# Optimization experiments

Measured on AMD Instinct MI355X. Metric: run time of the kernel, lower is better.

The kernel has to match this reference:

```python
import jax, jax.numpy as jnp
import numpy as np

DIM = 128; D_STATE = 16; D_CONV = 4; EXPAND = 2
D_INNER = DIM * EXPAND            # 256
DT_RANK = (DIM + 15) // 16        # 8
B, H, W = 2, 56, 56


def _ln(x, w, b):
    m = jnp.mean(x, -1, keepdims=True)
    v = jnp.var(x, -1, keepdims=True)
    return (x - m) * jax.lax.rsqrt(v + 1e-5) * w + b


def _mamba(x, in_w, conv_w, conv_b, xproj_w, dt_w, dt_b, A_log, Dp, out_w):
    # x: (B, L, DIM)
    Bb, L, _ = x.shape
    xz = x @ in_w.T                                   # (B,L,2*D_INNER)
    xi, z = jnp.split(xz, 2, axis=-1)
    # causal depthwise conv1d (pad left d_conv-1, truncate to L)
    xc = jnp.transpose(xi, (0, 2, 1))                 # (B,D_INNER,L)
    xc = jax.lax.conv_general_dilated(
        xc, conv_w, (1,), [(D_CONV - 1, 0)],
        dimension_numbers=('NCH', 'OIH', 'NCH'),
        feature_group_count=D_INNER) + conv_b[None, :, None]
    xs = jax.nn.silu(jnp.transpose(xc, (0, 2, 1)))    # (B,L,D_INNER)
    dbl = xs @ xproj_w.T                              # (B,L,DT_RANK+2*D_STATE)
    dt = jax.nn.softplus(dbl[..., :DT_RANK] @ dt_w.T + dt_b)   # (B,L,D_INNER)
    Bc = dbl[..., DT_RANK:DT_RANK + D_STATE]          # (B,L,D_STATE)
    Cc = dbl[..., DT_RANK + D_STATE:]                 # (B,L,D_STATE)
    A = -jnp.exp(A_log)                               # (D_INNER,D_STATE)
    dA = jnp.exp(dt[..., None] * A)                   # (B,L,D_INNER,D_STATE)
    dBu = (dt * xs)[..., None] * Bc[:, :, None, :]    # (B,L,D_INNER,D_STATE)

    def step(h, inp):
        a, bu, c = inp
        h = a * h + bu                                # (B,D_INNER,D_STATE)
        return h, jnp.einsum('bdn,bn->bd', h, c)

    h0 = jnp.zeros((Bb, D_INNER, D_STATE), x.dtype)
    _, ys = jax.lax.scan(step, h0, (jnp.moveaxis(dA, 1, 0),
                                    jnp.moveaxis(dBu, 1, 0),
                                    jnp.moveaxis(Cc, 1, 0)))
    y = jnp.moveaxis(ys, 0, 1) + xs * Dp              # (B,L,D_INNER)
    y = y * jax.nn.silu(z)
    return y @ out_w.T                                # (B,L,DIM)


def _forward(x, norm_h_w, norm_h_b, norm_v_w, norm_v_b,
             dw_w, dw_b, pw_w, pw_b,
             h_in_w, h_conv_w, h_conv_b, h_xproj_w, h_dt_w, h_dt_b, h_A_log, h_D, h_out_w,
             v_in_w, v_conv_w, v_conv_b, v_xproj_w, v_dt_w, v_dt_b, v_A_log, v_D, v_out_w,
             ca_fc1_w, ca_fc2_w):
    Bb, C, Hh, Ww = x.shape
    # local branch: depthwise 3x3 + GELU + 1x1
    lf = jax.lax.conv_general_dilated(
        x, dw_w, (1, 1), [(1, 1), (1, 1)],
        dimension_numbers=('NCHW', 'OIHW', 'NCHW'),
        feature_group_count=C) + dw_b[None, :, None, None]
    lf = jax.nn.gelu(lf, approximate=False)
    lf = jnp.einsum('bchw,oc->bohw', lf, pw_w[:, :, 0, 0]) + pw_b[None, :, None, None]
    # horizontal scan: row-major tokens
    xh = _ln(x.reshape(Bb, C, Hh * Ww).transpose(0, 2, 1), norm_h_w, norm_h_b)
    oh = _mamba(xh, h_in_w, h_conv_w, h_conv_b, h_xproj_w, h_dt_w, h_dt_b,
                h_A_log, h_D, h_out_w)
    oh = oh.transpose(0, 2, 1).reshape(Bb, C, Hh, Ww)
    # vertical scan: column-major tokens
    xv = _ln(jnp.transpose(x, (0, 1, 3, 2)).reshape(Bb, C, Ww * Hh).transpose(0, 2, 1),
             norm_v_w, norm_v_b)
    ov = _mamba(xv, v_in_w, v_conv_w, v_conv_b, v_xproj_w, v_dt_w, v_dt_b,
                v_A_log, v_D, v_out_w)
    ov = jnp.transpose(ov.transpose(0, 2, 1).reshape(Bb, C, Ww, Hh), (0, 1, 3, 2))
    fused = oh + ov + lf
    # channel attention
    y = jnp.mean(fused, axis=(2, 3))                  # (B,C)
    y = jax.nn.sigmoid(jax.nn.relu(y @ ca_fc1_w.T) @ ca_fc2_w.T)
    return fused * y[:, :, None, None] + x


def setup_inputs() -> dict:
    key = jax.random.key(0)
    ks = iter(jax.random.split(key, 64))
    def nrm(shape, scale):
        return jax.random.normal(next(ks), shape, jnp.float32) * scale
    d = {}
    d['x'] = nrm((B, DIM, H, W), 1.0)
    d['norm_h_w'] = jnp.ones((DIM,), jnp.float32); d['norm_h_b'] = jnp.zeros((DIM,), jnp.float32)
    d['norm_v_w'] = jnp.ones((DIM,), jnp.float32); d['norm_v_b'] = jnp.zeros((DIM,), jnp.float32)
    d['dw_w'] = nrm((DIM, 1, 3, 3), 1.0 / 3.0)
    d['dw_b'] = jnp.zeros((DIM,), jnp.float32)
    d['pw_w'] = nrm((DIM, DIM, 1, 1), DIM ** -0.5)
    d['pw_b'] = jnp.zeros((DIM,), jnp.float32)
    for p in ('h', 'v'):
        d[p + '_in_w'] = nrm((2 * D_INNER, DIM), DIM ** -0.5)
        d[p + '_conv_w'] = nrm((D_INNER, 1, D_CONV), D_CONV ** -0.5)
        d[p + '_conv_b'] = jnp.zeros((D_INNER,), jnp.float32)
        d[p + '_xproj_w'] = nrm((DT_RANK + 2 * D_STATE, D_INNER), D_INNER ** -0.5)
        d[p + '_dt_w'] = nrm((D_INNER, DT_RANK), DT_RANK ** -0.5)
        d[p + '_dt_b'] = jnp.full((D_INNER,), -2.0, jnp.float32)  # small positive dt
        d[p + '_A_log'] = jnp.log(jnp.tile(jnp.arange(1, D_STATE + 1, dtype=jnp.float32), (D_INNER, 1)))
        d[p + '_D'] = jnp.ones((D_INNER,), jnp.float32)
        d[p + '_out_w'] = nrm((DIM, D_INNER), D_INNER ** -0.5)
    d['ca_fc1_w'] = nrm((DIM // 4, DIM), DIM ** -0.5)
    d['ca_fc2_w'] = nrm((DIM, DIM // 4), (DIM // 4) ** -0.5)
    return d


def reference(x, norm_h_w, norm_h_b, norm_v_w, norm_v_b,
              dw_w, dw_b, pw_w, pw_b,
              h_in_w, h_conv_w, h_conv_b, h_xproj_w, h_dt_w, h_dt_b, h_A_log, h_D, h_out_w,
              v_in_w, v_conv_w, v_conv_b, v_xproj_w, v_dt_w, v_dt_b, v_A_log, v_D, v_out_w,
              ca_fc1_w, ca_fc2_w):
    return _forward(x, norm_h_w, norm_h_b, norm_v_w, norm_v_b,
                    dw_w, dw_b, pw_w, pw_b,
                    h_in_w, h_conv_w, h_conv_b, h_xproj_w, h_dt_w, h_dt_b, h_A_log, h_D, h_out_w,
                    v_in_w, v_conv_w, v_conv_b, v_xproj_w, v_dt_w, v_dt_b, v_A_log, v_D, v_out_w,
                    ca_fc1_w, ca_fc2_w)
```

## Files before the change

### kernel.cpp

```cpp
#include <hip/hip_runtime.h>
#include <hip/hip_bf16.h>

typedef __hip_bfloat16 bf16;
__device__ __forceinline__ float b2f(bf16 v){ return __bfloat162float(v); }
__device__ __forceinline__ bf16 f2b(float v){ return __float2bfloat16(v); }

typedef __attribute__((ext_vector_type(8))) short frag_ab;
typedef __attribute__((ext_vector_type(4))) float frag_cd;
typedef __attribute__((ext_vector_type(4))) short short4v;

__device__ __forceinline__ frag_ab ld_frag_2xb64(const bf16* p){
  union { frag_ab f; short4v h[2]; } u;
  u.h[0] = *reinterpret_cast<const short4v*>(p);
  u.h[1] = *reinterpret_cast<const short4v*>(p+4);
  return u.f;
}

#define LLEN 3136
#define BATCH 2
#define NCHUNK 49
#define LC 64

__global__ void k_dwconv_gelu(const float* __restrict__ x, const float* __restrict__ dww,
                              const float* __restrict__ dwb, bf16* __restrict__ tmp){
  int bc = blockIdx.x;
  int c = bc & 127;
  const float* xp = x + (size_t)bc*LLEN;
  float w[9];
  #pragma unroll
  for (int i=0;i<9;i++) w[i] = dww[c*9+i];
  float bias = dwb[c];
  for (int p = threadIdx.x; p < LLEN; p += blockDim.x){
    int i = p/56, j = p%56;
    float acc = bias;
    #pragma unroll
    for (int a=0;a<3;a++){
      int ii = i + a - 1;
      if (ii < 0 || ii >= 56) continue;
      #pragma unroll
      for (int bb=0;bb<3;bb++){
        int jj = j + bb - 1;
        if (jj < 0 || jj >= 56) continue;
        acc += w[a*3+bb] * xp[ii*56+jj];
      }
    }
    float g = 0.5f*acc*(1.0f + erff(acc*0.70710678118654752f));
    tmp[(size_t)bc*LLEN + p] = f2b(g);
  }
}

__global__ void k_pw_gemm(const bf16* __restrict__ tmp, const float* __restrict__ pww,
                          const float* __restrict__ pwb, float* __restrict__ fused){
  int b  = blockIdx.z;
  int p0 = blockIdx.x * 64;
  int m0 = blockIdx.y * 64;
  const bf16* T = tmp + (size_t)b*128*LLEN;
  __shared__ __align__(16) bf16 sA[64][136];
  __shared__ __align__(16) bf16 sBt[64][132];
  int tid = threadIdx.x;
  #pragma unroll
  for (int r=0;r<8;r++){
    int idx = tid + r*256;
    int row = idx >> 5, c4 = (idx & 31)*4;
    float4 w4 = *reinterpret_cast<const float4*>(&pww[(size_t)(m0+row)*128 + c4]);
    bf16 t4[4] = {f2b(w4.x), f2b(w4.y), f2b(w4.z), f2b(w4.w)};
    *reinterpret_cast<double*>(&sA[row][c4]) = *reinterpret_cast<double*>(t4);
  }
  #pragma unroll
  for (int r=0;r<8;r++){
    int idx = tid + r*256;
    int c = idx >> 4, p4 = (idx & 15)*4;
    union { double d; bf16 v[4]; } u;
    u.d = *reinterpret_cast<const double*>(&T[(size_t)c*LLEN + p0 + p4]);
    #pragma unroll
    for (int j=0;j<4;j++) sBt[p4+j][c] = u.v[j];
  }
  __syncthreads();
  int wv2 = tid >> 6, lane = tid & 63;
  int qd = lane >> 4, mr = lane & 15;
  frag_cd acc[4] = {};
  #pragma unroll
  for (int k0=0;k0<128;k0+=32){
    frag_ab af = *reinterpret_cast<frag_ab*>(&sA[wv2*16+mr][k0+qd*8]);
    #pragma unroll
    for (int t=0;t<4;t++){
      frag_ab bfr = ld_frag_2xb64(&sBt[t*16+mr][k0+qd*8]);
      acc[t] = __builtin_amdgcn_mfma_f32_16x16x32_bf16(af, bfr, acc[t], 0, 0, 0);
    }
  }
  #pragma unroll
  for (int t=0;t<4;t++)
    #pragma unroll
    for (int r=0;r<4;r++){
      int m = m0 + wv2*16 + qd*4 + r;
      int p = p0 + t*16 + mr;
      fused[((size_t)b*128 + m)*LLEN + p] = acc[t][r] + pwb[m];
    }
}

__global__ void k_ln(const float* __restrict__ x, const float* nhw_, const float* nhb_,
                     const float* nvw_, const float* nvb_, bf16* __restrict__ xln){
  __shared__ float sx[128][57];
  __shared__ float smean[56], srstd[56];
  __shared__ float wh[128], bh[128], wv_[128], bv_[128];
  int h = blockIdx.x; int b = blockIdx.y;
  int tid = threadIdx.x;
  if (tid < 128){ wh[tid]=nhw_[tid]; bh[tid]=nhb_[tid];
                  wv_[tid]=nvw_[tid]; bv_[tid]=nvb_[tid]; }
  for (int idx = tid; idx < 128*56; idx += 256){
    int c = idx / 56, w = idx % 56;
    sx[c][w] = x[((size_t)(b*128+c))*LLEN + h*56 + w];
  }
  __syncthreads();
  if (tid < 56){
    float s=0.f, s2=0.f;
    for (int c=0;c<128;c++){ float v = sx[c][tid]; s+=v; s2+=v*v; }
    float m = s*(1.f/128.f);
    float var = s2*(1.f/128.f) - m*m;
    smean[tid]=m; srstd[tid]=rsqrtf(var+1e-5f);
  }
  __syncthreads();
  bf16* outh = xln;
  bf16* outv = xln + (size_t)BATCH*LLEN*128;
  for (int idx = tid; idx < 56*128; idx += 256){
    int w = idx >> 7, c = idx & 127;
    float v = (sx[c][w]-smean[w])*srstd[w];
    outh[((size_t)b*LLEN + h*56 + w)*128 + c] = f2b(v*wh[c]+bh[c]);
    outv[((size_t)b*LLEN + w*56 + h)*128 + c] = f2b(v*wv_[c]+bv_[c]);
  }
}

__global__ void k_inproj(const bf16* __restrict__ xln, const float* __restrict__ hw,
                         const float* __restrict__ vw, bf16* __restrict__ XI, bf16* __restrict__ Z){
  int dir = blockIdx.z;
  const bf16* A = xln + (size_t)dir*BATCH*LLEN*128;
  const float* W = dir ? vw : hw;
  int m0 = blockIdx.x*64, n0 = blockIdx.y*64;
  __shared__ __align__(16) bf16 sA[64][136];
  __shared__ __align__(16) bf16 sW[64][136];
  int tid = threadIdx.x;
  #pragma unroll
  for (int r=0;r<4;r++){
    int idx = tid + r*256;
    int row = idx >> 4, c8 = (idx & 15)*8;
    *reinterpret_cast<float4*>(&sA[row][c8]) =
        *reinterpret_cast<const float4*>(&A[(size_t)(m0+row)*128 + c8]);
  }
  #pragma unroll
  for (int r=0;r<8;r++){
    int idx = tid + r*256;
    int row = idx >> 5, c4 = (idx & 31)*4;
    float4 w4 = *reinterpret_cast<const float4*>(&W[(size_t)(n0+row)*128 + c4]);
    bf16 t4[4] = {f2b(w4.x), f2b(w4.y), f2b(w4.z), f2b(w4.w)};
    *reinterpret_cast<double*>(&sW[row][c4]) = *reinterpret_cast<double*>(t4);
  }
  __syncthreads();
  int wv2 = tid >> 6, lane = tid & 63;
  int qd = lane >> 4, mr = lane & 15;
  frag_cd acc[4] = {};
  #pragma unroll
  for (int k0=0;k0<128;k0+=32){
    frag_ab af = *reinterpret_cast<frag_ab*>(&sA[wv2*16+mr][k0+qd*8]);
    #pragma unroll
    for (int t=0;t<4;t++){
      frag_ab bfr = *reinterpret_cast<frag_ab*>(&sW[t*16+mr][k0+qd*8]);
      acc[t] = __builtin_amdgcn_mfma_f32_16x16x32_bf16(af, bfr, acc[t], 0, 0, 0);
    }
  }
  bf16* dst = (n0 < 256) ? XI : Z;
  int nb = n0 & 255;
  size_t dslab = (size_t)dir*BATCH*LLEN*256;
  #pragma unroll
  for (int t=0;t<4;t++)
    #pragma unroll
    for (int r=0;r<4;r++){
      int row = m0 + wv2*16 + qd*4 + r;
      int col = nb + t*16 + mr;
      dst[dslab + (size_t)row*256 + col] = f2b(acc[t][r]);
    }
}

__global__ void k_conv(const bf16* __restrict__ XI, const float* hw, const float* hb,
                       const float* vw, const float* vb, bf16* __restrict__ XS2){
  int dir = blockIdx.z;
  int b = blockIdx.y;
  int bd = dir*BATCH + b;
  int l0 = blockIdx.x * 32;
  const bf16* XId = XI + (size_t)bd*LLEN*256;
  const float* cw = dir ? vw : hw;
  const float* cb = dir ? vb : hb;
  __shared__ float sxi[35][256];
  int tid = threadIdx.x;
  for (int r = 0; r < 35; r++){
    int l = l0 - 3 + r;
    sxi[r][tid] = (l >= 0) ? b2f(XId[(size_t)l*256 + tid]) : 0.f;
  }
  __syncthreads();
  float w0=cw[tid*4], w1=cw[tid*4+1], w2=cw[tid*4+2], w3=cw[tid*4+3];
  float bias = cb[tid];
  size_t x2base = ((size_t)bd*16 + (tid>>4))*LLEN;
  int c16 = tid & 15;
  for (int ll=0; ll<32; ll++){
    float acc = bias + w0*sxi[ll][tid] + w1*sxi[ll+1][tid] + w2*sxi[ll+2][tid] + w3*sxi[ll+3][tid];
    float s = acc / (1.f + __expf(-acc));
    XS2[(x2base + l0 + ll)*16 + c16] = f2b(s);
  }
}

__global__ void k_dbl(const bf16* __restrict__ XS2, const float* __restrict__ hx,
                      const float* __restrict__ vx,
                      const float* hdw, const float* vdw, const float* hdb, const float* vdb,
                      bf16* __restrict__ DT2, float* __restrict__ Bf, float* __restrict__ Cf){
  int m0 = blockIdx.x*64;
  int bd = m0 / LLEN;
  int l0m = m0 % LLEN;
  int dirq = bd >> 1;
  const float* W = dirq ? vx : hx;
  __shared__ __align__(16) bf16 sA[64][264];
  __shared__ __align__(16) bf16 sW[48][264];
  __shared__ float sdbl[64][49];
  int tid = threadIdx.x;
  #pragma unroll
  for (int r=0;r<8;r++){
    int idx = tid + r*256;
    int row = idx >> 5, c8 = (idx & 31)*8;
    size_t src = (((size_t)bd*16 + (c8>>4))*LLEN + l0m + row)*16 + (c8&15);
    *reinterpret_cast<float4*>(&sA[row][c8]) =
        *reinterpret_cast<const float4*>(&XS2[src]);
  }
  #pragma unroll
  for (int r=0;r<12;r++){
    int idx = tid + r*256;
    int row = idx >> 6, c4 = (idx & 63)*4;
    bf16 t4[4] = {f2b(0.f), f2b(0.f), f2b(0.f), f2b(0.f)};
    if (row < 40){
      float4 w4 = *reinterpret_cast<const float4*>(&W[(size_t)row*256 + c4]);
      t4[0]=f2b(w4.x); t4[1]=f2b(w4.y); t4[2]=f2b(w4.z); t4[3]=f2b(w4.w);
    }
    *reinterpret_cast<double*>(&sW[row][c4]) = *reinterpret_cast<double*>(t4);
  }
  __syncthreads();
  int wv2 = tid >> 6, lane = tid & 63;
  int qd = lane >> 4, mr = lane & 15;
  frag_cd acc[3] = {};
  #pragma unroll
  for (int k0=0;k0<256;k0+=32){
    frag_ab af = *reinterpret_cast<frag_ab*>(&sA[wv2*16+mr][k0+qd*8]);
    #pragma unroll
    for (int t=0;t<3;t++){
      frag_ab bfr = *reinterpret_cast<frag_ab*>(&sW[t*16+mr][k0+qd*8]);
      acc[t] = __builtin_amdgcn_mfma_f32_16x16x32_bf16(af, bfr, acc[t], 0, 0, 0);
    }
  }
  #pragma unroll
  for (int t=0;t<3;t++)
    #pragma unroll
    for (int r=0;r<4;r++){
      int col = t*16 + mr;
      if (col < 40) sdbl[wv2*16 + qd*4 + r][col] = acc[t][r];
    }
  __syncthreads();
  const float* dtw = dirq ? vdw : hdw;
  const float* dtb = dirq ? vdb : hdb;
  float w8[8];
  #pragma unroll
  for (int r=0;r<8;r++) w8[r] = dtw[tid*8+r];
  float biasv = dtb[tid];
  size_t d2base = ((size_t)bd*16 + (tid>>4))*LLEN + l0m;
  int c16 = tid & 15;
  for (int row=0; row<64; row++){
    float a = biasv;
    #pragma unroll
    for (int r=0;r<8;r++) a += sdbl[row][r]*w8[r];
    float sv = (a > 20.f) ? a : __logf(1.f + __expf(a));
    DT2[(d2base + row)*16 + c16] = f2b(sv);
  }
  #pragma unroll
  for (int r=0;r<8;r++){
    int idx = tid + r*256;
    int row = idx >> 5, o = idx & 31;
    float v = sdbl[row][8+o];
    size_t rr = (size_t)(m0+row)*16;
    if (o < 16) Bf[rr + o] = v;
    else        Cf[rr + (o-16)] = v;
  }
}

__global__ void k_scan1(const bf16* __restrict__ DT2, const bf16* __restrict__ XS2,
                        const float* __restrict__ Bc, const float* hA, const float* vA,
                        float* __restrict__ Pbuf, float* __restrict__ Hbuf){
  int bd = blockIdx.z;
  int g  = blockIdx.y;
  int ck = blockIdx.x;
  int l0 = ck*LC;
  const float* Bd = Bc + (size_t)bd*LLEN*16;
  const float* Alog = (bd >> 1) ? vA : hA;
  int tid = threadIdx.x;
  int dl = tid >> 4, n = tid & 15;
  int d = g*16 + dl;
  float A = -__expf(Alog[d*16+n]);
  __shared__ float sdt[LC][16], sxs[LC][16], sB[LC][16];
  size_t base2 = (((size_t)bd*16 + g)*LLEN + l0)*16;
  #pragma unroll
  for (int r=0;r<4;r++){
    int idx = tid + r*256;
    sdt[idx>>4][idx&15] = b2f(DT2[base2 + idx]);
    sxs[idx>>4][idx&15] = b2f(XS2[base2 + idx]);
    (&sB[0][0])[idx] = Bd[(size_t)l0*16 + idx];
  }
  __syncthreads();
  float h = 0.f, P = 1.f;
  #pragma unroll 8
  for (int i=0;i<LC;i++){
    float a = sdt[i][dl];
    float u = sxs[i][dl];
    float dA = __expf(a * A);
    h = dA*h + (a*u)*sB[i][n];
    P *= dA;
  }
  size_t sidx = (((size_t)bd*16 + g)*NCHUNK + ck)*256 + tid;
  Pbuf[sidx] = P;
  Hbuf[sidx] = h;
}

__global__ void k_scan2(const float* __restrict__ Pbuf, float* __restrict__ Hbuf){
  int q = blockIdx.x;
  int tid = threadIdx.x;
  float carry = 0.f;
  for (int k=0;k<NCHUNK;k++){
    size_t idx = ((size_t)q*NCHUNK + k)*256 + tid;
    float Pv = Pbuf[idx];
    float He = Hbuf[idx];
    Hbuf[idx] = carry;
    carry = Pv*carry + He;
  }
}

__global__ void k_scan3(const bf16* __restrict__ DT2, const bf16* __restrict__ XS2,
                        const float* __restrict__ Bc, const float* __restrict__ Cc,
                        const float* hA, const float* vA,
                        const float* __restrict__ Hbuf, bf16* __restrict__ ys){
  int bd = blockIdx.z;
  int g  = blockIdx.y;
  int ck = blockIdx.x;
  int l0 = ck*LC;
  const float* Bd = Bc + (size_t)bd*LLEN*16;
  const float* Cd = Cc + (size_t)bd*LLEN*16;
  bf16* yd = ys + (size_t)bd*LLEN*256;
  const float* Alog = (bd >> 1) ? vA : hA;
  int tid = threadIdx.x;
  int dl = tid >> 4, n = tid & 15;
  float A = -__expf(Alog[(g*16+dl)*16+n]);
  __shared__ float sdt[LC][16], sxs[LC][16], sB[LC][16], sC[LC][16];
  __shared__ __align__(16) float sp2[16][276];
  size_t base2 = (((size_t)bd*16 + g)*LLEN + l0)*16;
  #pragma unroll
  for (int r=0;r<4;r++){
    int idx = tid + r*256;
    sdt[idx>>4][idx&15] = b2f(DT2[base2 + idx]);
    sxs[idx>>4][idx&15] = b2f(XS2[base2 + idx]);
    (&sB[0][0])[idx] = Bd[(size_t)l0*16 + idx];
    (&sC[0][0])[idx] = Cd[(size_t)l0*16 + idx];
  }
  size_t sidx = (((size_t)bd*16 + g)*NCHUNK + ck)*256 + tid;
  float h = Hbuf[sidx];
  __syncthreads();
  int i_local = tid >> 4;
  int c16 = tid & 15;
  for (int i0=0; i0<LC; i0+=16){
    #pragma unroll
    for (int ii=0;ii<16;ii++){
      int i = i0 + ii;
      float a = sdt[i][dl];
      float u = sxs[i][dl];
      float dA = __expf(a * A);
      h = dA*h + (a*u)*sB[i][n];
      sp2[ii][tid] = h * sC[i][n];
    }
    __syncthreads();
    const float* row = &sp2[i_local][c16*16];
    float s = 0.f;
    #pragma unroll
    for (int k=0;k<4;k++){
      float4 v = *reinterpret_cast<const float4*>(row + k*4);
      s += v.x + v.y + v.z + v.w;
    }
    yd[(size_t)(l0+i0+i_local)*256 + g*16 + c16] = f2b(s);
    __syncthreads();
  }
}

__global__ void k_outgemm(const bf16* __restrict__ ys, const bf16* __restrict__ XS2,
                          const bf16* __restrict__ Z, const float* __restrict__ hD,
                          const float* __restrict__ vD, const float* __restrict__ how,
                          const float* __restrict__ vow, bf16* __restrict__ OD){
  int dir = blockIdx.z;
  size_t slab = (size_t)dir*BATCH*LLEN*256;
  const float* W = dir ? vow : how;
  const float* Dw = dir ? vD : hD;
  bf16* od = OD + (size_t)dir*BATCH*LLEN*128;
  int m0 = blockIdx.x*64, n0 = blockIdx.y*64;
  int bd = dir*2 + m0/LLEN;
  int lbase = m0 % LLEN;
  __shared__ __align__(16) bf16 sA[64][136];
  __shared__ __align__(16) bf16 sW[64][136];
  int tid = threadIdx.x;
  int wv2 = tid >> 6, lane = tid & 63;
  int qd = lane >> 4, mr = lane & 15;
  frag_cd acc[4] = {};
  for (int kc=0; kc<256; kc+=128){
    __syncthreads();
    #pragma unroll
    for (int r=0;r<4;r++){
      int idx = tid + r*256;
      int row = idx >> 4, c8 = (idx & 15)*8;
      int k = kc + c8;
      size_t e = slab + (size_t)(m0+row)*256 + k;
      size_t e2 = (((size_t)bd*16 + (k>>4))*LLEN + lbase + row)*16 + (k&15);
      bf16 yb[8], xb[8], zb[8], ob[8];
      *reinterpret_cast<float4*>(yb) = *reinterpret_cast<const float4*>(&ys[e]);
      *reinterpret_cast<float4*>(xb) = *reinterpret_cast<const float4*>(&XS2[e2]);
      *reinterpret_cast<float4*>(zb) = *reinterpret_cast<const float4*>(&Z[e]);
      #pragma unroll
      for (int j=0;j<8;j++){
        float Dv = Dw[k + j];
        float yv = b2f(yb[j]) + b2f(xb[j])*Dv;
        float zv = b2f(zb[j]);
        ob[j] = f2b(yv * (zv/(1.f+__expf(-zv))));
      }
      *reinterpret_cast<float4*>(&sA[row][c8]) = *reinterpret_cast<float4*>(ob);
    }
    #pragma unroll
    for (int r=0;r<8;r++){
      int idx = tid + r*256;
      int row = idx >> 5, c4 = (idx & 31)*4;
      float4 w4 = *reinterpret_cast<const float4*>(&W[(size_t)(n0+row)*256 + kc + c4]);
      bf16 t4[4] = {f2b(w4.x), f2b(w4.y), f2b(w4.z), f2b(w4.w)};
      *reinterpret_cast<double*>(&sW[row][c4]) = *reinterpret_cast<double*>(t4);
    }
    __syncthreads();
    #pragma unroll
    for (int k0=0;k0<128;k0+=32){
      frag_ab af = *reinterpret_cast<frag_ab*>(&sA[wv2*16+mr][k0+qd*8]);
      #pragma unroll
      for (int t=0;t<4;t++){
        frag_ab bfr = *reinterpret_cast<frag_ab*>(&sW[t*16+mr][k0+qd*8]);
        acc[t] = __builtin_amdgcn_mfma_f32_16x16x32_bf16(af, bfr, acc[t], 0, 0, 0);
      }
    }
  }
  #pragma unroll
  for (int t=0;t<4;t++)
    #pragma unroll
    for (int r=0;r<4;r++){
      int row = m0 + wv2*16 + qd*4 + r;
      int col = n0 + t*16 + mr;
      od[(size_t)row*128 + col] = f2b(acc[t][r]);
    }
}

__global__ void k_combine(const bf16* __restrict__ OD, float* __restrict__ fused,
                          float* __restrict__ BSUM){
  int h = blockIdx.x;
  int b = blockIdx.y;
  __shared__ float sfu[56][129];
  int tid = threadIdx.x;
  const bf16* od0 = OD + (size_t)b*LLEN*128;
  const bf16* od1 = OD + (size_t)(BATCH + b)*LLEN*128;
  #pragma unroll 4
  for (int it=0; it<28; it++){
    int idx = it*256 + tid;
    int sp = idx >> 7, c = idx & 127;
    sfu[sp][c] = b2f(od0[(size_t)(h*56+sp)*128 + c]) + b2f(od1[(size_t)(sp*56+h)*128 + c]);
  }
  __syncthreads();
  int c = tid >> 1, half = tid & 1;
  float s = 0.f;
  size_t gbase = ((size_t)b*128 + c)*LLEN + h*56 + half*28;
  #pragma unroll
  for (int i=0;i<28;i++){
    float tot = fused[gbase+i] + sfu[half*28+i][c];
    fused[gbase+i] = tot;
    s += tot;
  }
  s += __shfl_xor(s, 1, 64);
  if (half == 0) BSUM[((size_t)b*56 + h)*128 + c] = s;
}

__global__ void k_gate(const float* __restrict__ BSUM, const float* fc1, const float* fc2,
                       float* __restrict__ gate){
  int b = blockIdx.x;
  __shared__ float ym[128], s1[32];
  int tid = threadIdx.x;
  float s = 0.f;
  for (int h=0; h<56; h++) s += BSUM[((size_t)b*56 + h)*128 + tid];
  ym[tid] = s * (1.f/(float)LLEN);
  __syncthreads();
  if (tid < 32){
    float a = 0.f;
    for (int c=0;c<128;c++) a += ym[c]*fc1[tid*128+c];
    s1[tid] = fmaxf(a, 0.f);
  }
  __syncthreads();
  float a = 0.f;
  #pragma unroll
  for (int j=0;j<32;j++) a += s1[j]*fc2[tid*32+j];
  gate[b*128+tid] = 1.f/(1.f+__expf(-a));
}

__global__ void k_final(float* __restrict__ fused, const float* __restrict__ gate,
                        const float* __restrict__ x, float* __restrict__ out){
  int i = blockIdx.x*256 + threadIdx.x;
  if (i >= BATCH*128*LLEN) return;
  int bc = i / LLEN;
  float v = fused[i]*gate[bc] + x[i];
  out[i] = v;
}

extern "C" void kernel_launch(void* const* d_in, const int* in_sizes, int n_in,
                              void* d_out, int out_size, void* d_ws, size_t ws_size,
                              hipStream_t stream) {
  const float* x      = (const float*)d_in[0];
  const float* nhw    = (const float*)d_in[1];
  const float* nhb    = (const float*)d_in[2];
  const float* nvw    = (const float*)d_in[3];
  const float* nvb    = (const float*)d_in[4];
  const float* dww    = (const float*)d_in[5];
  const float* dwb    = (const float*)d_in[6];
  const float* pww    = (const float*)d_in[7];
  const float* pwb    = (const float*)d_in[8];
  const float* h_inw  = (const float*)d_in[9];
  const float* h_cw   = (const float*)d_in[10];
  const float* h_cb   = (const float*)d_in[11];
  const float* h_xw   = (const float*)d_in[12];
  const float* h_dtw  = (const float*)d_in[13];
  const float* h_dtb  = (const float*)d_in[14];
  const float* h_Al   = (const float*)d_in[15];
  const float* h_D    = (const float*)d_in[16];
  const float* h_ow   = (const float*)d_in[17];
  const float* v_inw  = (const float*)d_in[18];
  const float* v_cw   = (const float*)d_in[19];
  const float* v_cb   = (const float*)d_in[20];
  const float* v_xw   = (const float*)d_in[21];
  const float* v_dtw  = (const float*)d_in[22];
  const float* v_dtb  = (const float*)d_in[23];
  const float* v_Al   = (const float*)d_in[24];
  const float* v_D    = (const float*)d_in[25];
  const float* v_ow   = (const float*)d_in[26];
  const float* fc1    = (const float*)d_in[27];
  const float* fc2    = (const float*)d_in[28];

  float* FUSED = (float*)d_out;
  float* out   = (float*)d_out;

  char* base = (char*)d_ws;
  bf16*  TMP   = (bf16*)(base + 0);
  bf16*  XLN   = (bf16*)(base + 1605632);
  bf16*  DT2   = (bf16*)(base + 0);
  bf16*  OD    = (bf16*)(base + 0);
  bf16*  XI    = (bf16*)(base + 6422528);
  bf16*  YS    = (bf16*)(base + 6422528);
  float* Pbuf  = (float*)(base + 6422528);
  bf16*  Z     = (bf16*)(base + 12845056);
  bf16*  XS2   = (bf16*)(base + 19267584);
  float* Bf    = (float*)(base + 25690112);
  float* Cf    = (float*)(base + 26492928);
  float* Hbuf  = (float*)(base + 27295744);
  float* BSUM  = (float*)(base + 30507008);
  float* GATE  = (float*)(base + 30564352);

  k_dwconv_gelu<<<dim3(BATCH*128), dim3(256), 0, stream>>>(x, dww, dwb, TMP);
  k_pw_gemm<<<dim3(49,2,BATCH), dim3(256), 0, stream>>>(TMP, pww, pwb, FUSED);
  k_ln<<<dim3(56,BATCH), dim3(256), 0, stream>>>(x, nhw, nhb, nvw, nvb, XLN);
  k_inproj<<<dim3(98,8,2), dim3(256), 0, stream>>>(XLN, h_inw, v_inw, XI, Z);
  k_conv<<<dim3(98,BATCH,2), dim3(256), 0, stream>>>(XI, h_cw, h_cb, v_cw, v_cb, XS2);
  k_dbl<<<dim3(196), dim3(256), 0, stream>>>(XS2, h_xw, v_xw, h_dtw, v_dtw, h_dtb, v_dtb,
                                             DT2, Bf, Cf);
  k_scan1<<<dim3(NCHUNK,16,4), dim3(256), 0, stream>>>(DT2, XS2, Bf, h_Al, v_Al, Pbuf, Hbuf);
  k_scan2<<<dim3(64), dim3(256), 0, stream>>>(Pbuf, Hbuf);
  k_scan3<<<dim3(NCHUNK,16,4), dim3(256), 0, stream>>>(DT2, XS2, Bf, Cf, h_Al, v_Al, Hbuf, YS);
  k_outgemm<<<dim3(98,2,2), dim3(256), 0, stream>>>(YS, XS2, Z, h_D, v_D, h_ow, v_ow, OD);
  k_combine<<<dim3(56,BATCH), dim3(256), 0, stream>>>(OD, FUSED, BSUM);
  k_gate<<<dim3(BATCH), dim3(128), 0, stream>>>(BSUM, fc1, fc2, GATE);
  k_final<<<dim3((BATCH*128*LLEN+255)/256), dim3(256), 0, stream>>>(FUSED, GATE, x, out);
}
```

Before: 257.7 us.

## Fuse chunk scan pass into dbl kernel, split dwconv grid, atomic gate mean

Moves the first chunked selective-scan pass into the x-projection kernel so dt, u and B are consumed from shared memory without being re-read, and drops the separate scan1 launch. The depthwise conv gets four times more blocks by splitting the spatial range. The per-row channel sums for the gate are accumulated with atomics into a zeroed mean buffer instead of a separate partial-sum array. The fused scan runs each thread over 16 states serially, which reduces parallelism in that phase.

```diff
diff --git a/kernel.cpp b/kernel.cpp
--- a/kernel.cpp
+++ b/kernel.cpp
@@ -22,15 +22,19 @@
 #define LC 64
 
 __global__ void k_dwconv_gelu(const float* __restrict__ x, const float* __restrict__ dww,
-                              const float* __restrict__ dwb, bf16* __restrict__ tmp){
+                              const float* __restrict__ dwb, bf16* __restrict__ tmp,
+                              float* __restrict__ YMEAN){
   int bc = blockIdx.x;
   int c = bc & 127;
+  if (bc == 0 && blockIdx.y == 0 && threadIdx.x < 256) YMEAN[threadIdx.x] = 0.f;
   const float* xp = x + (size_t)bc*LLEN;
   float w[9];
   #pragma unroll
   for (int i=0;i<9;i++) w[i] = dww[c*9+i];
   float bias = dwb[c];
-  for (int p = threadIdx.x; p < LLEN; p += blockDim.x){
+  int pstart = blockIdx.y * 784;
+  int pend = pstart + 784;
+  for (int p = pstart + threadIdx.x; p < pend; p += 256){
     int i = p/56, j = p%56;
     float acc = bias;
     #pragma unroll
@@ -210,10 +214,13 @@
 __global__ void k_dbl(const bf16* __restrict__ XS2, const float* __restrict__ hx,
                       const float* __restrict__ vx,
                       const float* hdw, const float* vdw, const float* hdb, const float* vdb,
-                      bf16* __restrict__ DT2, float* __restrict__ Bf, float* __restrict__ Cf){
+                      const float* hA, const float* vA,
+                      bf16* __restrict__ DT2, float* __restrict__ Bf, float* __restrict__ Cf,
+                      float* __restrict__ Pbuf, float* __restrict__ Hbuf){
   int m0 = blockIdx.x*64;
   int bd = m0 / LLEN;
   int l0m = m0 % LLEN;
+  int ck = l0m / LC;
   int dirq = bd >> 1;
   const float* W = dirq ? vx : hx;
   __shared__ __align__(16) bf16 sA[64][264];
@@ -262,10 +269,18 @@
   __syncthreads();
   const float* dtw = dirq ? vdw : hdw;
   const float* dtb = dirq ? vdb : hdb;
+  const float* Alog = dirq ? vA : hA;
   float w8[8];
   #pragma unroll
   for (int r=0;r<8;r++) w8[r] = dtw[tid*8+r];
   float biasv = dtb[tid];
+  float Aq[16];
+  #pragma unroll
+  for (int n=0;n<16;n++) Aq[n] = -__expf(Alog[tid*16+n]);
+  float hst[16] = {};
+  float Pst[16];
+  #pragma unroll
+  for (int n=0;n<16;n++) Pst[n] = 1.f;
   size_t d2base = ((size_t)bd*16 + (tid>>4))*LLEN + l0m;
   int c16 = tid & 15;
   for (int row=0; row<64; row++){
@@ -273,8 +288,21 @@
     #pragma unroll
     for (int r=0;r<8;r++) a += sdbl[row][r]*w8[r];
     float sv = (a > 20.f) ? a : __logf(1.f + __expf(a));
-    DT2[(d2base + row)*16 + c16] = f2b(sv);
-  }
+    bf16 svb16 = f2b(sv);
+    DT2[(d2base + row)*16 + c16] = svb16;
+    float svb = b2f(svb16);
+    float u = b2f(sA[row][tid]);
+    float au = svb*u;
+    #pragma unroll
+    for (int n=0;n<16;n++){
+      float dA = __expf(svb * Aq[n]);
+      hst[n] = dA*hst[n] + au*sdbl[row][8+n];
+      Pst[n] *= dA;
+    }
+  }
+  size_t pbase = (((size_t)bd*16 + (tid>>4))*NCHUNK + ck)*256 + (size_t)(tid&15)*16;
+  #pragma unroll
+  for (int n=0;n<16;n++){ Pbuf[pbase+n] = Pst[n]; Hbuf[pbase+n] = hst[n]; }
   #pragma unroll
   for (int r=0;r<8;r++){
     int idx = tid + r*256;
@@ -284,43 +312,6 @@
     if (o < 16) Bf[rr + o] = v;
     else        Cf[rr + (o-16)] = v;
   }
-}
-
-__global__ void k_scan1(const bf16* __restrict__ DT2, const bf16* __restrict__ XS2,
-                        const float* __restrict__ Bc, const float* hA, const float* vA,
-                        float* __restrict__ Pbuf, float* __restrict__ Hbuf){
-  int bd = blockIdx.z;
-  int g  = blockIdx.y;
-  int ck = blockIdx.x;
-  int l0 = ck*LC;
-  const float* Bd = Bc + (size_t)bd*LLEN*16;
-  const float* Alog = (bd >> 1) ? vA : hA;
-  int tid = threadIdx.x;
-  int dl = tid >> 4, n = tid & 15;
-  int d = g*16 + dl;
-  float A = -__expf(Alog[d*16+n]);
-  __shared__ float sdt[LC][16], sxs[LC][16], sB[LC][16];
-  size_t base2 = (((size_t)bd*16 + g)*LLEN + l0)*16;
-  #pragma unroll
-  for (int r=0;r<4;r++){
-    int idx = tid + r*256;
-    sdt[idx>>4][idx&15] = b2f(DT2[base2 + idx]);
-    sxs[idx>>4][idx&15] = b2f(XS2[base2 + idx]);
-    (&sB[0][0])[idx] = Bd[(size_t)l0*16 + idx];
-  }
-  __syncthreads();
-  float h = 0.f, P = 1.f;
-  #pragma unroll 8
-  for (int i=0;i<LC;i++){
-    float a = sdt[i][dl];
-    float u = sxs[i][dl];
-    float dA = __expf(a * A);
-    h = dA*h + (a*u)*sB[i][n];
-    P *= dA;
-  }
-  size_t sidx = (((size_t)bd*16 + g)*NCHUNK + ck)*256 + tid;
-  Pbuf[sidx] = P;
-  Hbuf[sidx] = h;
 }
 
 __global__ void k_scan2(const float* __restrict__ Pbuf, float* __restrict__ Hbuf){
@@ -460,7 +451,7 @@
 }
 
 __global__ void k_combine(const bf16* __restrict__ OD, float* __restrict__ fused,
-                          float* __restrict__ BSUM){
+                          float* __restrict__ YMEAN){
   int h = blockIdx.x;
   int b = blockIdx.y;
   __shared__ float sfu[56][129];
@@ -484,17 +475,15 @@
     s += tot;
   }
   s += __shfl_xor(s, 1, 64);
-  if (half == 0) BSUM[((size_t)b*56 + h)*128 + c] = s;
-}
-
-__global__ void k_gate(const float* __restrict__ BSUM, const float* fc1, const float* fc2,
+  if (half == 0) atomicAdd(&YMEAN[b*128 + c], s);
+}
+
+__global__ void k_gate(const float* __restrict__ YMEAN, const float* fc1, const float* fc2,
                        float* __restrict__ gate){
   int b = blockIdx.x;
   __shared__ float ym[128], s1[32];
   int tid = threadIdx.x;
-  float s = 0.f;
-  for (int h=0; h<56; h++) s += BSUM[((size_t)b*56 + h)*128 + tid];
-  ym[tid] = s * (1.f/(float)LLEN);
+  ym[tid] = YMEAN[b*128 + tid] * (1.f/(float)LLEN);
   __syncthreads();
   if (tid < 32){
     float a = 0.f;
@@ -566,21 +555,20 @@
   float* Bf    = (float*)(base + 25690112);
   float* Cf    = (float*)(base + 26492928);
   float* Hbuf  = (float*)(base + 27295744);
-  float* BSUM  = (float*)(base + 30507008);
+  float* YMEAN = (float*)(base + 30507008);
   float* GATE  = (float*)(base + 30564352);
 
-  k_dwconv_gelu<<<dim3(BATCH*128), dim3(256), 0, stream>>>(x, dww, dwb, TMP);
+  k_dwconv_gelu<<<dim3(BATCH*128,4), dim3(256), 0, stream>>>(x, dww, dwb, TMP, YMEAN);
   k_pw_gemm<<<dim3(49,2,BATCH), dim3(256), 0, stream>>>(TMP, pww, pwb, FUSED);
   k_ln<<<dim3(56,BATCH), dim3(256), 0, stream>>>(x, nhw, nhb, nvw, nvb, XLN);
   k_inproj<<<dim3(98,8,2), dim3(256), 0, stream>>>(XLN, h_inw, v_inw, XI, Z);
   k_conv<<<dim3(98,BATCH,2), dim3(256), 0, stream>>>(XI, h_cw, h_cb, v_cw, v_cb, XS2);
   k_dbl<<<dim3(196), dim3(256), 0, stream>>>(XS2, h_xw, v_xw, h_dtw, v_dtw, h_dtb, v_dtb,
-                                             DT2, Bf, Cf);
-  k_scan1<<<dim3(NCHUNK,16,4), dim3(256), 0, stream>>>(DT2, XS2, Bf, h_Al, v_Al, Pbuf, Hbuf);
+                                             h_Al, v_Al, DT2, Bf, Cf, Pbuf, Hbuf);
   k_scan2<<<dim3(64), dim3(256), 0, stream>>>(Pbuf, Hbuf);
   k_scan3<<<dim3(NCHUNK,16,4), dim3(256), 0, stream>>>(DT2, XS2, Bf, Cf, h_Al, v_Al, Hbuf, YS);
   k_outgemm<<<dim3(98,2,2), dim3(256), 0, stream>>>(YS, XS2, Z, h_D, v_D, h_ow, v_ow, OD);
-  k_combine<<<dim3(56,BATCH), dim3(256), 0, stream>>>(OD, FUSED, BSUM);
-  k_gate<<<dim3(BATCH), dim3(128), 0, stream>>>(BSUM, fc1, fc2, GATE);
+  k_combine<<<dim3(56,BATCH), dim3(256), 0, stream>>>(OD, FUSED, YMEAN);
+  k_gate<<<dim3(BATCH), dim3(128), 0, stream>>>(YMEAN, fc1, fc2, GATE);
   k_final<<<dim3((BATCH*128*LLEN+255)/256), dim3(256), 0, stream>>>(FUSED, GATE, x, out);
 }
```

Result: no change. 257.3 us (-0.1%).
